# Performance work log

Hardware: AMD Instinct MI355X
Metric: run time of the kernel (lower is better)

## Reference

```python
import jax, jax.numpy as jnp
import numpy as np

CLIP_VAL = 2.5
NUM_BITS = 8
LN_EPS = 1e-12


def _fake_quant_sym(x, clip_val=CLIP_VAL, num_bits=NUM_BITS):
    """Symmetric layerwise fake quantization with straight-through estimator.

    clamp -> per-tensor scale from max|x| -> round -> dequant. The STE trick
    (x + stop_grad(q - x)) makes the forward value equal to the quantized
    value while the gradient passes through the clamp only.
    """
    qmax = float(2 ** (num_bits - 1) - 1)
    xc = jnp.clip(x, -clip_val, clip_val)
    s = qmax / jnp.maximum(jnp.max(jnp.abs(xc)), 1e-8)
    q = jnp.round(xc * s) / s
    return xc + jax.lax.stop_gradient(q - xc)


def setup_inputs() -> dict:
    key = jax.random.key(0)
    ks = jax.random.split(key, 4)
    B, S, H = 8, 4096, 1024
    return {
        "hidden_states": jax.random.normal(ks[0], (B, S, H), dtype=jnp.float32),
        "input_tensor": jax.random.normal(ks[1], (B, S, H), dtype=jnp.float32),
        "weight": jax.random.normal(ks[2], (H, H), dtype=jnp.float32) * 0.02,
        "bias": jax.random.normal(ks[3], (H,), dtype=jnp.float32) * 0.02,
        "ln_gamma": jnp.ones((H,), dtype=jnp.float32),
        "ln_beta": jnp.zeros((H,), dtype=jnp.float32),
    }


def reference(hidden_states, input_tensor, weight, bias, ln_gamma, ln_beta):
    # QuantizeLinear: fake-quant activations and weight, then GEMM + bias.
    hq = _fake_quant_sym(hidden_states)
    wq = _fake_quant_sym(weight)
    h = jnp.einsum("bsh,oh->bso", hq, wq) + bias  # [B, S, H]
    # Dropout is identity in eval mode. Residual + LayerNorm over last dim.
    y = h + input_tensor
    mu = jnp.mean(y, axis=-1, keepdims=True)
    var = jnp.mean(jnp.square(y - mu), axis=-1, keepdims=True)
    y_norm = (y - mu) * jax.lax.rsqrt(var + LN_EPS)
    return y_norm * ln_gamma + ln_beta
```

## Files before the change

### kernel.cpp

```cpp
#include <hip/hip_runtime.h>
#include <hip/hip_bf16.h>
#include <stdint.h>

#define H_DIM 1024
#define QMAX 127.0f
#define CLIP 2.5f

typedef __attribute__((ext_vector_type(4))) float f32x4;
typedef __attribute__((ext_vector_type(4))) int i32x4;
typedef __attribute__((ext_vector_type(8))) short bf16x8;
typedef __attribute__((ext_vector_type(8))) unsigned short u16x8;
typedef __attribute__((address_space(3))) void lds_void;
typedef const __attribute__((address_space(1))) void gmem_void;

__device__ __forceinline__ unsigned short quant_bf16(float x, float s) {
  const float q = rintf(fminf(fmaxf(x, -CLIP), CLIP) * s);
  return (unsigned short)(__float_as_uint(q) >> 16);
}

__device__ __forceinline__ int quant_i8(float x, float s) {
  return (int)rintf(fminf(fmaxf(x, -CLIP), CLIP) * s);
}

__device__ __forceinline__ unsigned short f2bf_rne(float f) {
  const unsigned u = __float_as_uint(f);
  return (unsigned short)((u + 0x7FFFu + ((u >> 16) & 1u)) >> 16);
}

__device__ __forceinline__ float bf2f(unsigned short u) {
  return __uint_as_float((unsigned)u << 16);
}

__device__ __forceinline__ unsigned pack4_i8(float4 v, float s) {
  return ((unsigned)(unsigned char)(signed char)quant_i8(v.x, s)) |
         ((unsigned)(unsigned char)(signed char)quant_i8(v.y, s) << 8) |
         ((unsigned)(unsigned char)(signed char)quant_i8(v.z, s) << 16) |
         ((unsigned)(unsigned char)(signed char)quant_i8(v.w, s) << 24);
}

__global__ __launch_bounds__(256) void absmax_clip_kernel(
    const float* __restrict__ x, long n, float* __restrict__ out) {
  float m = 0.f;
  const long stride = (long)gridDim.x * blockDim.x * 4;
  for (long i = ((long)blockIdx.x * blockDim.x + threadIdx.x) * 4; i < n; i += stride) {
    const float4 v = *reinterpret_cast<const float4*>(x + i);
    m = fmaxf(m, fmaxf(fmaxf(fabsf(v.x), fabsf(v.y)), fmaxf(fabsf(v.z), fabsf(v.w))));
  }
  m = fminf(m, CLIP);
#pragma unroll
  for (int off = 32; off > 0; off >>= 1) m = fmaxf(m, __shfl_down(m, off));
  __shared__ float red[4];
  const int lane = threadIdx.x & 63, w = threadIdx.x >> 6;
  if (lane == 0) red[w] = m;
  __syncthreads();
  if (threadIdx.x == 0) {
    const float mm = fmaxf(fmaxf(red[0], red[1]), fmaxf(red[2], red[3]));
    atomicMax(reinterpret_cast<unsigned int*>(out), __float_as_uint(mm));
  }
}

__global__ __launch_bounds__(256) void quant_kernel(
    const float* __restrict__ x, unsigned short* __restrict__ q,
    const float* __restrict__ amax_p, long n) {
  const float s = QMAX / fmaxf(amax_p[0], 1e-8f);
  const long stride = (long)gridDim.x * blockDim.x * 4;
  for (long i = ((long)blockIdx.x * blockDim.x + threadIdx.x) * 4; i < n; i += stride) {
    const float4 v = *reinterpret_cast<const float4*>(x + i);
    ushort4 o;
    o.x = quant_bf16(v.x, s);
    o.y = quant_bf16(v.y, s);
    o.z = quant_bf16(v.z, s);
    o.w = quant_bf16(v.w, s);
    *reinterpret_cast<ushort4*>(q + i) = o;
  }
}

__global__ __launch_bounds__(256) void quant8_kernel(
    const float* __restrict__ x, signed char* __restrict__ q,
    const float* __restrict__ amax_p, long n) {
  const float s = QMAX / fmaxf(amax_p[0], 1e-8f);
  const long stride = (long)gridDim.x * blockDim.x * 8;
  for (long i = ((long)blockIdx.x * blockDim.x + threadIdx.x) * 8; i < n; i += stride) {
    const float4 v0 = *reinterpret_cast<const float4*>(x + i);
    const float4 v1 = *reinterpret_cast<const float4*>(x + i + 4);
    uint2 o; o.x = pack4_i8(v0, s); o.y = pack4_i8(v1, s);
    *reinterpret_cast<uint2*>(q + i) = o;
  }
}

#define BMs 128
#define BNs 128
#define BKs8 64
#define NIT8 (H_DIM / BKs8)

__global__ __launch_bounds__(256) void gemm_s8_kernel(
    const signed char* __restrict__ Aq8, const signed char* __restrict__ Wq8,
    const float* __restrict__ bias, const float* __restrict__ scales,
    unsigned short* __restrict__ gbf, int M) {
  __shared__ __attribute__((aligned(16))) char SM8[81920];
  char* As = SM8;
  char* Bs = SM8 + 40960;

  const int nwg = (M / BMs) * 8;
  const int orig = blockIdx.x;
  const int cpx = nwg >> 3;
  const int wg = ((nwg & 7) == 0) ? ((orig & 7) * cpx + (orig >> 3)) : orig;
  const int bn = wg & 7, bm = wg >> 3;
  const int m0 = bm * BMs, n0 = bn * BNs;

  const int t = threadIdx.x;
  const int lane = t & 63, wid = t >> 6;
  const int wr = wid >> 1, wc = wid & 1;
  const int lrow = lane & 15, lgrp = lane >> 4;

  const float amax_h = fmaxf(scales[0], 1e-8f);
  const float amax_w = fmaxf(scales[1], 1e-8f);
  const float inv_s = (amax_h * amax_w) / (QMAX * QMAX);

  const int c0 = t, c1 = t + 256;
  const int r0 = c0 >> 2, r1 = c1 >> 2;
  const unsigned g0 = (unsigned)r0 * H_DIM + (unsigned)((((c0 & 3) ^ ((r0 >> 1) & 3))) * 16);
  const unsigned g1 = (unsigned)r1 * H_DIM + (unsigned)((((c1 & 3) ^ ((r1 >> 1) & 3))) * 16);
  const signed char* Ag = Aq8 + (size_t)m0 * H_DIM;
  const signed char* Bg = Wq8 + (size_t)n0 * H_DIM;

#define STAGE_T8(BUF, KQ)                                                      \
  { __builtin_amdgcn_global_load_lds((gmem_void*)(Ag + g0 + (KQ)),             \
        (lds_void*)(As + (BUF)*8192 + c0 * 16), 16, 0, 0);                     \
    __builtin_amdgcn_global_load_lds((gmem_void*)(Ag + g1 + (KQ)),             \
        (lds_void*)(As + (BUF)*8192 + c1 * 16), 16, 0, 0);                     \
    __builtin_amdgcn_global_load_lds((gmem_void*)(Bg + g0 + (KQ)),             \
        (lds_void*)(Bs + (BUF)*8192 + c0 * 16), 16, 0, 0);                     \
    __builtin_amdgcn_global_load_lds((gmem_void*)(Bg + g1 + (KQ)),             \
        (lds_void*)(Bs + (BUF)*8192 + c1 * 16), 16, 0, 0); }

  int offA[4], offB[4];
#pragma unroll
  for (int i = 0; i < 4; ++i) {
    const int r = wr * 64 + i * 16 + lrow;
    offA[i] = r * 64 + ((lgrp ^ ((r >> 1) & 3)) * 16);
  }
#pragma unroll
  for (int j = 0; j < 4; ++j) {
    const int r = wc * 64 + j * 16 + lrow;
    offB[j] = r * 64 + ((lgrp ^ ((r >> 1) & 3)) * 16);
  }

  i32x4 acc[4][4];
#pragma unroll
  for (int i = 0; i < 4; i++)
#pragma unroll
    for (int j = 0; j < 4; j++)
#pragma unroll
      for (int r = 0; r < 4; r++) acc[i][j][r] = 0;

  STAGE_T8(0, 0)
  STAGE_T8(1, BKs8)
  STAGE_T8(2, 2 * BKs8)
  STAGE_T8(3, 3 * BKs8)

  for (int it = 0; it < NIT8; ++it) {
    const int cb = it % 5;
    if (it <= NIT8 - 4) {
      asm volatile("s_waitcnt vmcnt(12)" ::: "memory");
    } else if (it == NIT8 - 3) {
      asm volatile("s_waitcnt vmcnt(8)" ::: "memory");
    } else if (it == NIT8 - 2) {
      asm volatile("s_waitcnt vmcnt(4)" ::: "memory");
    } else {
      asm volatile("s_waitcnt vmcnt(0)" ::: "memory");
    }
    __builtin_amdgcn_s_barrier();

    i32x4 af[4], bfr[4];
#pragma unroll
    for (int i = 0; i < 4; ++i)
      af[i] = *reinterpret_cast<const i32x4*>(As + cb * 8192 + offA[i]);
#pragma unroll
    for (int j = 0; j < 4; ++j)
      bfr[j] = *reinterpret_cast<const i32x4*>(Bs + cb * 8192 + offB[j]);
    __builtin_amdgcn_s_setprio(1);
#pragma unroll
    for (int i = 0; i < 4; ++i)
#pragma unroll
      for (int j = 0; j < 4; ++j)
        acc[i][j] = __builtin_amdgcn_mfma_i32_16x16x64_i8(af[i], bfr[j], acc[i][j], 0, 0, 0);
    __builtin_amdgcn_s_setprio(0);

    if (it + 4 < NIT8) {
      STAGE_T8((it + 4) % 5, (unsigned)((it + 4) * BKs8))
    }
  }
#undef STAGE_T8
  __syncthreads();

  unsigned short* SMu = reinterpret_cast<unsigned short*>(SM8);
#pragma unroll
  for (int j = 0; j < 4; ++j) {
    const int cl = wc * 64 + j * 16 + lrow;
    const float bv = bias[n0 + cl];
#pragma unroll
    for (int i = 0; i < 4; ++i) {
      const int rl0 = wr * 64 + i * 16 + lgrp * 4;
#pragma unroll
      for (int r = 0; r < 4; ++r)
        SMu[(rl0 + r) * 136 + cl] = f2bf_rne((float)acc[i][j][r] * inv_s + bv);
    }
  }
  __syncthreads();
  {
    const int e_row = t >> 1, e_half = t & 1;
    unsigned short* dst = gbf + (size_t)(m0 + e_row) * H_DIM + n0 + e_half * 64;
    const unsigned short* src = SMu + e_row * 136 + e_half * 64;
#pragma unroll
    for (int c = 0; c < 8; ++c)
      *reinterpret_cast<u16x8*>(dst + c * 8) =
          *reinterpret_cast<const u16x8*>(src + c * 8);
  }
}

__global__ __launch_bounds__(256) void ln_resid_kernel(
    const unsigned short* __restrict__ gbf, const float* __restrict__ resid,
    const float* __restrict__ gamma, const float* __restrict__ beta,
    float* __restrict__ out) {
  const int rl = threadIdx.x >> 7;
  const int c0 = (threadIdx.x & 127) * 8;
  const size_t base = ((size_t)blockIdx.x * 2 + rl) * H_DIM + c0;

  const u16x8 g = *reinterpret_cast<const u16x8*>(gbf + base);
  const float4 rA = *reinterpret_cast<const float4*>(resid + base);
  const float4 rB = *reinterpret_cast<const float4*>(resid + base + 4);
  float v[8];
  v[0] = bf2f(g[0]) + rA.x; v[1] = bf2f(g[1]) + rA.y;
  v[2] = bf2f(g[2]) + rA.z; v[3] = bf2f(g[3]) + rA.w;
  v[4] = bf2f(g[4]) + rB.x; v[5] = bf2f(g[5]) + rB.y;
  v[6] = bf2f(g[6]) + rB.z; v[7] = bf2f(g[7]) + rB.w;

  float s = 0.f, ss = 0.f;
#pragma unroll
  for (int k = 0; k < 8; ++k) { s += v[k]; ss += v[k] * v[k]; }
#pragma unroll
  for (int off = 32; off > 0; off >>= 1) {
    s += __shfl_down(s, off);
    ss += __shfl_down(ss, off);
  }
  __shared__ float red[4][2];
  const int lane = threadIdx.x & 63, w = threadIdx.x >> 6;
  if (lane == 0) { red[w][0] = s; red[w][1] = ss; }
  __syncthreads();
  const int wp = rl * 2;
  const float stot = red[wp][0] + red[wp + 1][0];
  const float sstot = red[wp][1] + red[wp + 1][1];
  const float mu = stot * (1.0f / H_DIM);
  const float var = fmaxf(sstot * (1.0f / H_DIM) - mu * mu, 0.f);
  const float rs = rsqrtf(var + 1e-12f);

  const float4 gA = *reinterpret_cast<const float4*>(gamma + c0);
  const float4 gB = *reinterpret_cast<const float4*>(gamma + c0 + 4);
  const float4 bA = *reinterpret_cast<const float4*>(beta + c0);
  const float4 bB = *reinterpret_cast<const float4*>(beta + c0 + 4);
  float4 oA, oB;
  oA.x = (v[0] - mu) * rs * gA.x + bA.x;
  oA.y = (v[1] - mu) * rs * gA.y + bA.y;
  oA.z = (v[2] - mu) * rs * gA.z + bA.z;
  oA.w = (v[3] - mu) * rs * gA.w + bA.w;
  oB.x = (v[4] - mu) * rs * gB.x + bB.x;
  oB.y = (v[5] - mu) * rs * gB.y + bB.y;
  oB.z = (v[6] - mu) * rs * gB.z + bB.z;
  oB.w = (v[7] - mu) * rs * gB.w + bB.w;
  *reinterpret_cast<float4*>(out + base) = oA;
  *reinterpret_cast<float4*>(out + base + 4) = oB;
}

#define BM 128
#define BN 128
#define BK 32

__global__ __launch_bounds__(256, 2) void gemm_fused_kernel(
    const float* __restrict__ A, const unsigned short* __restrict__ Wq,
    const float* __restrict__ bias, const float* __restrict__ resid,
    const float* __restrict__ scales, float* __restrict__ out, int M) {
  __shared__ unsigned short Asf[BM][40];
  __shared__ unsigned short Bsf[BN][40];
  const int nbm = M / BM;
  const int bm = blockIdx.x % nbm, bn = blockIdx.x / nbm;
  const int m0 = bm * BM, n0 = bn * BN;
  const int t = threadIdx.x;
  const int lane = t & 63, wid = t >> 6;
  const int wr = wid >> 1, wc = wid & 1;
  const int lrow = lane & 15, lgrp = lane >> 4;
  const float amax_h = fmaxf(scales[0], 1e-8f);
  const float amax_w = fmaxf(scales[1], 1e-8f);
  const float sh = QMAX / amax_h;
  const float inv_s = (amax_h * amax_w) / (QMAX * QMAX);
  f32x4 acc[4][4];
#pragma unroll
  for (int i = 0; i < 4; i++)
#pragma unroll
    for (int j = 0; j < 4; j++)
#pragma unroll
      for (int r = 0; r < 4; r++) acc[i][j][r] = 0.f;
  for (int k0 = 0; k0 < H_DIM; k0 += BK) {
#pragma unroll
    for (int j = 0; j < 4; ++j) {
      const int f = j * 256 + t;
      const int r = f >> 3, c4 = f & 7;
      const float4 v = *reinterpret_cast<const float4*>(A + (size_t)(m0 + r) * H_DIM + k0 + c4 * 4);
      ushort4 q;
      q.x = quant_bf16(v.x, sh); q.y = quant_bf16(v.y, sh);
      q.z = quant_bf16(v.z, sh); q.w = quant_bf16(v.w, sh);
      *reinterpret_cast<ushort4*>(&Asf[r][c4 * 4]) = q;
    }
#pragma unroll
    for (int j = 0; j < 2; ++j) {
      const int f = j * 256 + t;
      const int r = f >> 2, cb = f & 3;
      const uint4 v = *reinterpret_cast<const uint4*>(Wq + (size_t)(n0 + r) * H_DIM + k0 + cb * 8);
      *reinterpret_cast<uint4*>(&Bsf[r][cb * 8]) = v;
    }
    __syncthreads();
    bf16x8 af[4], bfr[4];
#pragma unroll
    for (int i = 0; i < 4; i++)
      af[i] = *reinterpret_cast<const bf16x8*>(&Asf[wr * 64 + i * 16 + lrow][lgrp * 8]);
#pragma unroll
    for (int j = 0; j < 4; j++)
      bfr[j] = *reinterpret_cast<const bf16x8*>(&Bsf[wc * 64 + j * 16 + lrow][lgrp * 8]);
#pragma unroll
    for (int i = 0; i < 4; i++)
#pragma unroll
      for (int j = 0; j < 4; j++)
        acc[i][j] = __builtin_amdgcn_mfma_f32_16x16x32_bf16(af[i], bfr[j], acc[i][j], 0, 0, 0);
    __syncthreads();
  }
#pragma unroll
  for (int j = 0; j < 4; j++) {
    const int col = n0 + wc * 64 + j * 16 + lrow;
    const float bv = bias[col];
#pragma unroll
    for (int i = 0; i < 4; i++) {
      const int row0 = m0 + wr * 64 + i * 16 + lgrp * 4;
#pragma unroll
      for (int r = 0; r < 4; r++) {
        const size_t off = (size_t)(row0 + r) * H_DIM + col;
        out[off] = acc[i][j][r] * inv_s + bv + resid[off];
      }
    }
  }
}

__global__ __launch_bounds__(256) void ln_kernel(
    float* __restrict__ y, const float* __restrict__ gamma,
    const float* __restrict__ beta) {
  const size_t base = (size_t)blockIdx.x * H_DIM + threadIdx.x * 4;
  const float4 v = *reinterpret_cast<const float4*>(y + base);
  float s = v.x + v.y + v.z + v.w;
  float ss = v.x * v.x + v.y * v.y + v.z * v.z + v.w * v.w;
#pragma unroll
  for (int off = 32; off > 0; off >>= 1) {
    s += __shfl_down(s, off);
    ss += __shfl_down(ss, off);
  }
  __shared__ float red[8];
  const int lane = threadIdx.x & 63, w = threadIdx.x >> 6;
  if (lane == 0) { red[w] = s; red[4 + w] = ss; }
  __syncthreads();
  const float stot = red[0] + red[1] + red[2] + red[3];
  const float sstot = red[4] + red[5] + red[6] + red[7];
  const float mu = stot * (1.0f / H_DIM);
  const float var = fmaxf(sstot * (1.0f / H_DIM) - mu * mu, 0.f);
  const float rs = rsqrtf(var + 1e-12f);
  const float4 g = *reinterpret_cast<const float4*>(gamma + threadIdx.x * 4);
  const float4 b = *reinterpret_cast<const float4*>(beta + threadIdx.x * 4);
  float4 o;
  o.x = (v.x - mu) * rs * g.x + b.x;
  o.y = (v.y - mu) * rs * g.y + b.y;
  o.z = (v.z - mu) * rs * g.z + b.z;
  o.w = (v.w - mu) * rs * g.w + b.w;
  *reinterpret_cast<float4*>(y + base) = o;
}

extern "C" void kernel_launch(void* const* d_in, const int* in_sizes, int n_in,
                              void* d_out, int out_size, void* d_ws, size_t ws_size,
                              hipStream_t stream) {
  const float* hidden = (const float*)d_in[0];
  const float* resid  = (const float*)d_in[1];
  const float* weight = (const float*)d_in[2];
  const float* bias   = (const float*)d_in[3];
  const float* gamma  = (const float*)d_in[4];
  const float* beta   = (const float*)d_in[5];
  float* out = (float*)d_out;

  const long nh = (long)in_sizes[0];
  const int M = (int)(nh / H_DIM);
  const long nw = (long)H_DIM * H_DIM;

  float* scales = (float*)d_ws;
  char* base = (char*)d_ws + 256;
  signed char* Wq8 = (signed char*)base;
  signed char* Aq8 = (signed char*)(base + nw);
  unsigned short* gbf = (unsigned short*)(base + nw + nh);
  const size_t need1 = 256 + (size_t)nw + (size_t)nh * 3;
  const size_t need3 = 256 + (size_t)nw * 2;

  hipMemsetAsync(d_ws, 0, 8, stream);

  if (ws_size >= need1 && (M % BMs) == 0 && (M % 2) == 0 && (nh % 8) == 0) {
    absmax_clip_kernel<<<2048, 256, 0, stream>>>(hidden, nh, scales + 0);
    absmax_clip_kernel<<<256, 256, 0, stream>>>(weight, nw, scales + 1);
    quant8_kernel<<<512, 256, 0, stream>>>(weight, Wq8, scales + 1, nw);
    quant8_kernel<<<2048, 256, 0, stream>>>(hidden, Aq8, scales + 0, nh);
    gemm_s8_kernel<<<(M / BMs) * (H_DIM / BNs), 256, 0, stream>>>(
        Aq8, Wq8, bias, scales, gbf, M);
    ln_resid_kernel<<<M / 2, 256, 0, stream>>>(gbf, resid, gamma, beta, out);
  } else if (ws_size >= need3 && (M % BM) == 0) {
    unsigned short* Wqf = (unsigned short*)base;
    absmax_clip_kernel<<<2048, 256, 0, stream>>>(hidden, nh, scales + 0);
    absmax_clip_kernel<<<256, 256, 0, stream>>>(weight, nw, scales + 1);
    quant_kernel<<<1024, 256, 0, stream>>>(weight, Wqf, scales + 1, nw);
    gemm_fused_kernel<<<(M / BM) * (H_DIM / BN), 256, 0, stream>>>(
        hidden, Wqf, bias, resid, scales, out, M);
    ln_kernel<<<M, 256, 0, stream>>>(out, gamma, beta);
  }
}
```

Measured before the change: 199.2 us.

## Switch int8 GEMM to BK=128 double-buffered pipeline with 8-way LDS swizzle

The int8 GEMM K-step goes from 64 to 128, and the 5-stage, 4-deep prefetch ring is replaced by a 2-buffer scheme. The next tile is issued at the top of each iteration, and a second barrier at the end guards buffer reuse. The LDS swizzle is widened to 8 slots per 128-byte row, and each iteration runs two 64-wide k sub-steps. The aim is to halve loop iterations and cut LDS from 80KB to 64KB, which may allow more resident workgroups, at the cost of shallower prefetch depth and an extra barrier per iteration.

```diff
diff --git a/kernel.cpp b/kernel.cpp
--- a/kernel.cpp
+++ b/kernel.cpp
@@ -90,16 +90,16 @@
 
 #define BMs 128
 #define BNs 128
-#define BKs8 64
+#define BKs8 128
 #define NIT8 (H_DIM / BKs8)
 
 __global__ __launch_bounds__(256) void gemm_s8_kernel(
     const signed char* __restrict__ Aq8, const signed char* __restrict__ Wq8,
     const float* __restrict__ bias, const float* __restrict__ scales,
     unsigned short* __restrict__ gbf, int M) {
-  __shared__ __attribute__((aligned(16))) char SM8[81920];
+  __shared__ __attribute__((aligned(16))) char SM8[65536];
   char* As = SM8;
-  char* Bs = SM8 + 40960;
+  char* Bs = SM8 + 32768;
 
   const int nwg = (M / BMs) * 8;
   const int orig = blockIdx.x;
@@ -117,33 +117,38 @@
   const float amax_w = fmaxf(scales[1], 1e-8f);
   const float inv_s = (amax_h * amax_w) / (QMAX * QMAX);
 
-  const int c0 = t, c1 = t + 256;
-  const int r0 = c0 >> 2, r1 = c1 >> 2;
-  const unsigned g0 = (unsigned)r0 * H_DIM + (unsigned)((((c0 & 3) ^ ((r0 >> 1) & 3))) * 16);
-  const unsigned g1 = (unsigned)r1 * H_DIM + (unsigned)((((c1 & 3) ^ ((r1 >> 1) & 3))) * 16);
+  unsigned gsrc[4];
+  int ldst[4];
+#pragma unroll
+  for (int j = 0; j < 4; ++j) {
+    const int c = t + 256 * j;
+    const int row = c >> 3, slot = c & 7;
+    gsrc[j] = (unsigned)row * H_DIM + (unsigned)(((slot ^ (row & 7))) * 16);
+    ldst[j] = c * 16;
+  }
   const signed char* Ag = Aq8 + (size_t)m0 * H_DIM;
   const signed char* Bg = Wq8 + (size_t)n0 * H_DIM;
 
 #define STAGE_T8(BUF, KQ)                                                      \
-  { __builtin_amdgcn_global_load_lds((gmem_void*)(Ag + g0 + (KQ)),             \
-        (lds_void*)(As + (BUF)*8192 + c0 * 16), 16, 0, 0);                     \
-    __builtin_amdgcn_global_load_lds((gmem_void*)(Ag + g1 + (KQ)),             \
-        (lds_void*)(As + (BUF)*8192 + c1 * 16), 16, 0, 0);                     \
-    __builtin_amdgcn_global_load_lds((gmem_void*)(Bg + g0 + (KQ)),             \
-        (lds_void*)(Bs + (BUF)*8192 + c0 * 16), 16, 0, 0);                     \
-    __builtin_amdgcn_global_load_lds((gmem_void*)(Bg + g1 + (KQ)),             \
-        (lds_void*)(Bs + (BUF)*8192 + c1 * 16), 16, 0, 0); }
+  { _Pragma("unroll")                                                          \
+    for (int j = 0; j < 4; ++j)                                                \
+      __builtin_amdgcn_global_load_lds((gmem_void*)(Ag + gsrc[j] + (KQ)),      \
+          (lds_void*)(As + (BUF)*16384 + ldst[j]), 16, 0, 0);                  \
+    _Pragma("unroll")                                                          \
+    for (int j = 0; j < 4; ++j)                                                \
+      __builtin_amdgcn_global_load_lds((gmem_void*)(Bg + gsrc[j] + (KQ)),      \
+          (lds_void*)(Bs + (BUF)*16384 + ldst[j]), 16, 0, 0); }
 
   int offA[4], offB[4];
 #pragma unroll
   for (int i = 0; i < 4; ++i) {
     const int r = wr * 64 + i * 16 + lrow;
-    offA[i] = r * 64 + ((lgrp ^ ((r >> 1) & 3)) * 16);
+    offA[i] = r * 128 + ((lgrp ^ (r & 7)) * 16);
   }
 #pragma unroll
   for (int j = 0; j < 4; ++j) {
     const int r = wc * 64 + j * 16 + lrow;
-    offB[j] = r * 64 + ((lgrp ^ ((r >> 1) & 3)) * 16);
+    offB[j] = r * 128 + ((lgrp ^ (r & 7)) * 16);
   }
 
   i32x4 acc[4][4];
@@ -155,41 +160,37 @@
       for (int r = 0; r < 4; r++) acc[i][j][r] = 0;
 
   STAGE_T8(0, 0)
-  STAGE_T8(1, BKs8)
-  STAGE_T8(2, 2 * BKs8)
-  STAGE_T8(3, 3 * BKs8)
 
   for (int it = 0; it < NIT8; ++it) {
-    const int cb = it % 5;
-    if (it <= NIT8 - 4) {
-      asm volatile("s_waitcnt vmcnt(12)" ::: "memory");
-    } else if (it == NIT8 - 3) {
+    const int cur = it & 1, nxt = cur ^ 1;
+    if (it + 1 < NIT8) {
+      STAGE_T8(nxt, (unsigned)((it + 1) * BKs8))
       asm volatile("s_waitcnt vmcnt(8)" ::: "memory");
-    } else if (it == NIT8 - 2) {
-      asm volatile("s_waitcnt vmcnt(4)" ::: "memory");
     } else {
       asm volatile("s_waitcnt vmcnt(0)" ::: "memory");
     }
     __builtin_amdgcn_s_barrier();
-
-    i32x4 af[4], bfr[4];
-#pragma unroll
-    for (int i = 0; i < 4; ++i)
-      af[i] = *reinterpret_cast<const i32x4*>(As + cb * 8192 + offA[i]);
-#pragma unroll
-    for (int j = 0; j < 4; ++j)
-      bfr[j] = *reinterpret_cast<const i32x4*>(Bs + cb * 8192 + offB[j]);
-    __builtin_amdgcn_s_setprio(1);
-#pragma unroll
-    for (int i = 0; i < 4; ++i)
+    __builtin_amdgcn_sched_barrier(0);
+
+#pragma unroll
+    for (int ks = 0; ks < 2; ++ks) {
+      i32x4 af[4], bfr[4];
+      const int kx = ks * 64;
+#pragma unroll
+      for (int i = 0; i < 4; ++i)
+        af[i] = *reinterpret_cast<const i32x4*>(As + cur * 16384 + (offA[i] ^ kx));
 #pragma unroll
       for (int j = 0; j < 4; ++j)
-        acc[i][j] = __builtin_amdgcn_mfma_i32_16x16x64_i8(af[i], bfr[j], acc[i][j], 0, 0, 0);
-    __builtin_amdgcn_s_setprio(0);
-
-    if (it + 4 < NIT8) {
-      STAGE_T8((it + 4) % 5, (unsigned)((it + 4) * BKs8))
-    }
+        bfr[j] = *reinterpret_cast<const i32x4*>(Bs + cur * 16384 + (offB[j] ^ kx));
+      __builtin_amdgcn_s_setprio(1);
+#pragma unroll
+      for (int i = 0; i < 4; ++i)
+#pragma unroll
+        for (int j = 0; j < 4; ++j)
+          acc[i][j] = __builtin_amdgcn_mfma_i32_16x16x64_i8(af[i], bfr[j], acc[i][j], 0, 0, 0);
+      __builtin_amdgcn_s_setprio(0);
+    }
+    __builtin_amdgcn_s_barrier();
   }
 #undef STAGE_T8
   __syncthreads();
```

Result: no change. 196.9 us (-1.2%).
